# Kernel tuning notes

Hardware: AMD Instinct MI355X
Metric: run time of the kernel (lower is better)

Reference implementation:

```python
import jax, jax.numpy as jnp
import numpy as np

NUM_EXPERTS = 64
TOP_K = 2
B, S, EMB, MLP = 4, 2048, 1024, 2048


def setup_inputs() -> dict:
    key = jax.random.key(0)
    k1, k2, k3, k4, k5 = jax.random.split(key, 5)
    inputs = jax.random.normal(k1, (B, S, EMB), dtype=jnp.float32)
    gate_kernel = jax.random.normal(k2, (EMB, NUM_EXPERTS), dtype=jnp.float32) / np.sqrt(EMB)
    w0 = jax.random.normal(k3, (NUM_EXPERTS, EMB, MLP), dtype=jnp.float32) / np.sqrt(EMB)
    w1 = jax.random.normal(k4, (NUM_EXPERTS, EMB, MLP), dtype=jnp.float32) / np.sqrt(EMB)
    wo = jax.random.normal(k5, (NUM_EXPERTS, MLP, EMB), dtype=jnp.float32) / np.sqrt(MLP)
    return {"inputs": inputs, "gate_kernel": gate_kernel, "w0": w0, "w1": w1, "wo": wo}


def reference(inputs, gate_kernel, w0, w1, wo):
    b, s, e = inputs.shape
    x = inputs.reshape(b * s, e)                                  # [T, E]
    # Router (DenseGeneral gate)
    gate_logits = jnp.einsum('te,ex->tx', x, gate_kernel)         # [T, X]
    # permute(): top-k gating + sort tokens by expert
    weights, selected = jax.lax.top_k(gate_logits, TOP_K)         # [T, K]
    weights = jax.nn.softmax(weights.astype(jnp.float32), axis=-1)
    flat_experts = selected.reshape(-1)                           # [T*K]
    sort_idx = jnp.argsort(flat_experts)                          # [T*K]
    token_idx = sort_idx // TOP_K
    sorted_x = jnp.take(x, token_idx, axis=0)                     # [T*K, E]
    group_sizes = jnp.bincount(flat_experts, length=NUM_EXPERTS).astype(jnp.int32)
    # grouped GEMMs (gated FFN: silu(x@w0) * (x@w1) @ wo)
    h0 = jax.lax.ragged_dot(sorted_x, w0, group_sizes)            # [T*K, M]
    h1 = jax.lax.ragged_dot(sorted_x, w1, group_sizes)            # [T*K, M]
    inter = jax.nn.silu(h0) * h1
    out_sorted = jax.lax.ragged_dot(inter, wo, group_sizes)       # [T*K, E]
    # unpermute(): restore token order, weighted combine over top-k
    unsorted = jnp.take(out_sorted, jnp.argsort(sort_idx), axis=0)
    per_tok = unsorted.reshape(b * s, TOP_K, e)
    out = jnp.einsum('BKE,BK->BE', per_tok.astype(jnp.float32), weights)
    return out.reshape(b, s, e)
```

## Files before the change

### kernel.cpp

```cpp
#include <hip/hip_runtime.h>
#include <hip/hip_bf16.h>
#include <math.h>

#define NTOK   8192
#define NEXP   64
#define EMBD   1024
#define MLPD   2048
#define TOPK   2
#define NFLAT  (NTOK * TOPK)
#define BKD    32
#define MAXCH  8

typedef __attribute__((ext_vector_type(4)))  float  f32x4;
typedef __attribute__((ext_vector_type(16))) float  f32x16;
typedef __attribute__((ext_vector_type(8)))  __bf16 bf16x8;

__device__ __forceinline__ void gl16(const void* g, void* lds_base) {
  __builtin_amdgcn_global_load_lds(
      (const __attribute__((address_space(1))) unsigned int*)g,
      (__attribute__((address_space(3))) unsigned int*)lds_base, 16, 0, 0);
}

#define OFF_COUNTS 0
#define OFF_BASE   256
#define OFF_RUN    512
#define OFF_EFLAT  1024
#define OFF_WFLAT  (1024 + 65536)
#define OFF_ROWTOK (1024 + 2 * 65536)
#define OFF_F2R    (1024 + 3 * 65536)
#define OFF_INTER  (1024 + 4 * 65536)
#define OFF_OS     (OFF_INTER + (size_t)NFLAT * MLPD * 2)
#define OFF_XB     OFF_OS
#define NEED_F32   (OFF_OS + (size_t)NFLAT * EMBD * 4)

__global__ __launch_bounds__(256) void cvt_x_k(const float* __restrict__ x,
                                               __bf16* __restrict__ xb) {
  size_t i = ((size_t)blockIdx.x * 256 + threadIdx.x) * 8;
  f32x4 f0 = *(const f32x4*)(x + i);
  f32x4 f1 = *(const f32x4*)(x + i + 4);
  bf16x8 v;
  #pragma unroll
  for (int q = 0; q < 4; ++q) { v[q] = (__bf16)f0[q]; v[4 + q] = (__bf16)f1[q]; }
  *(bf16x8*)(xb + i) = v;
}

__global__ __launch_bounds__(256) void router_topk(
    const float* __restrict__ x, const float* __restrict__ gk,
    int* __restrict__ e_flat, float* __restrict__ w_flat) {
  int t = blockIdx.x * 4 + (threadIdx.x >> 6);
  int l = threadIdx.x & 63;
  const float* xr = x + (size_t)t * EMBD;
  float acc = 0.f;
  #pragma unroll 8
  for (int i = 0; i < EMBD; ++i)
    acc = fmaf(xr[i], gk[i * NEXP + l], acc);
  float m = acc;
  for (int o = 32; o; o >>= 1) m = fmaxf(m, __shfl_xor(m, o));
  unsigned long long b1 = __ballot(acc == m);
  int i1 = __ffsll(b1) - 1;
  float v2 = (l == i1) ? -INFINITY : acc;
  float m2 = v2;
  for (int o = 32; o; o >>= 1) m2 = fmaxf(m2, __shfl_xor(m2, o));
  unsigned long long b2 = __ballot(v2 == m2);
  int i2 = __ffsll(b2) - 1;
  if (l == 0) {
    float e2 = expf(m2 - m);
    float inv = 1.f / (1.f + e2);
    e_flat[2 * t] = i1;  e_flat[2 * t + 1] = i2;
    w_flat[2 * t] = inv; w_flat[2 * t + 1] = e2 * inv;
  }
}

__global__ void hist_k(const int* __restrict__ ef, int* __restrict__ counts) {
  int j = blockIdx.x * 256 + threadIdx.x;
  if (j < NFLAT) atomicAdd(&counts[ef[j]], 1);
}

__global__ void scan_k(const int* __restrict__ counts, int* __restrict__ base) {
  if (threadIdx.x == 0) {
    int s = 0;
    for (int e = 0; e < NEXP; ++e) { base[e] = s; s += counts[e]; }
  }
}

__global__ void scatter_k(const int* __restrict__ ef, const int* __restrict__ base,
                          int* __restrict__ run, int* __restrict__ rowtok,
                          int* __restrict__ f2r) {
  int j = blockIdx.x * 256 + threadIdx.x;
  if (j < NFLAT) {
    int e = ef[j];
    int r = base[e] + atomicAdd(&run[e], 1);
    f2r[j] = r;
    rowtok[r] = j >> 1;
  }
}

__global__ __launch_bounds__(256, 2) void gemm1_k(
    const __bf16* __restrict__ xb, const float* __restrict__ w0,
    const float* __restrict__ w1, const int* __restrict__ counts,
    const int* __restrict__ base, const int* __restrict__ rowtok,
    __hip_bfloat16* __restrict__ inter) {
  int e = blockIdx.z;
  int Me = counts[e];
  int mc = blockIdx.y;
  if (mc * 128 >= Me) return;
  int rs = base[e];
  int nb = blockIdx.x * 64;
  int t = threadIdx.x;
  int wv = t >> 6, l = t & 63;
  int wr = wv >> 1, wc = wv & 1;
  int lo = l & 31, hi = l >> 5;

  __shared__ __bf16 A1[3][4096];
  __shared__ float  B1[3][4096];

  int rga = mc * 128 + wv * 32 + lo; rga = rga < Me ? rga : Me - 1;
  const __bf16* abase = xb + (size_t)rowtok[rs + rga] * EMBD + hi * 8;
  int bm = wv >> 1, bk0 = (wv & 1) * 16;
  const float* wsel = bm ? w1 : w0;
  const float* wbase = wsel + (size_t)e * EMBD * MLPD + nb + (l & 15) * 4 +
                       (size_t)(l >> 4) * MLPD;

  auto STAGE = [&](int ks, int buf) {
    int kk = ks * BKD;
    #pragma unroll
    for (int kh = 0; kh < 2; ++kh)
      gl16(abase + kk + kh * 16, &A1[buf][(wv * 2 + kh) * 512]);
    #pragma unroll
    for (int j = 0; j < 4; ++j)
      gl16(wbase + (size_t)(kk + bk0 + j * 4) * MLPD,
           &B1[buf][bm * 2048 + (bk0 + j * 4) * 64]);
  };

  f32x16 acc0[2], acc1[2];
  #pragma unroll
  for (int g = 0; g < 2; ++g)
    #pragma unroll
    for (int r = 0; r < 16; ++r) { acc0[g][r] = 0.f; acc1[g][r] = 0.f; }

  const int NT = EMBD / BKD;
  STAGE(0, 0);
  STAGE(1, 1);
  int bufR = 0, bufW = 2;
  for (int ks = 0; ks < NT; ++ks) {
    if (ks + 1 < NT) asm volatile("s_waitcnt vmcnt(6)" ::: "memory");
    else             asm volatile("s_waitcnt vmcnt(0)" ::: "memory");
    __builtin_amdgcn_sched_barrier(0);
    __builtin_amdgcn_s_barrier();
    if (ks + 2 < NT) STAGE(ks + 2, bufW);

    bf16x8 av[2][2];
    #pragma unroll
    for (int g = 0; g < 2; ++g)
      #pragma unroll
      for (int kh = 0; kh < 2; ++kh)
        av[g][kh] = *(const bf16x8*)&A1[bufR][((wr * 2 + g) * 2 + kh) * 512 + l * 8];
    float b[2][2][8];
    #pragma unroll
    for (int m = 0; m < 2; ++m)
      #pragma unroll
      for (int kh = 0; kh < 2; ++kh) {
        int bi = m * 2048 + (kh * 16 + hi * 8) * 64 + wc * 32 + lo;
        #pragma unroll
        for (int q = 0; q < 8; ++q) b[m][kh][q] = B1[bufR][bi + q * 64];
      }
    bf16x8 bv0[2], bv1[2];
    #pragma unroll
    for (int kh = 0; kh < 2; ++kh)
      #pragma unroll
      for (int q = 0; q < 8; ++q) {
        bv0[kh][q] = (__bf16)b[0][kh][q];
        bv1[kh][q] = (__bf16)b[1][kh][q];
      }
    #pragma unroll
    for (int kh = 0; kh < 2; ++kh)
      #pragma unroll
      for (int g = 0; g < 2; ++g) {
        acc0[g] = __builtin_amdgcn_mfma_f32_32x32x16_bf16(av[g][kh], bv0[kh], acc0[g], 0, 0, 0);
        acc1[g] = __builtin_amdgcn_mfma_f32_32x32x16_bf16(av[g][kh], bv1[kh], acc1[g], 0, 0, 0);
      }
    bufR = bufR == 2 ? 0 : bufR + 1;
    bufW = bufW == 2 ? 0 : bufW + 1;
  }

  #pragma unroll
  for (int g = 0; g < 2; ++g)
    #pragma unroll
    for (int r = 0; r < 16; ++r) {
      int rl = mc * 128 + wr * 64 + g * 32 + (r & 3) + 8 * (r >> 2) + 4 * hi;
      if (rl < Me) {
        float h0 = acc0[g][r], h1 = acc1[g][r];
        float s = h0 / (1.f + expf(-h0)) * h1;
        inter[(size_t)(rs + rl) * MLPD + nb + wc * 32 + lo] = (__hip_bfloat16)s;
      }
    }
}

template <typename OS_T>
__global__ __launch_bounds__(256, 3) void gemm2_k(
    const __hip_bfloat16* __restrict__ inter, const float* __restrict__ wo,
    const int* __restrict__ counts, const int* __restrict__ base,
    OS_T* __restrict__ os) {
  int e = blockIdx.z;
  int Me = counts[e];
  int mc = blockIdx.y;
  if (mc * 128 >= Me) return;
  int rs = base[e];
  int nb = blockIdx.x * 64;
  int t = threadIdx.x;
  int wv = t >> 6, l = t & 63;
  int wr = wv >> 1, wc = wv & 1;
  int lo = l & 31, hi = l >> 5;

  __shared__ __bf16 A2[3][4096];
  __shared__ float  B2[3][2048];

  int rga = mc * 128 + wv * 32 + lo; rga = rga < Me ? rga : Me - 1;
  const __bf16* abase = (const __bf16*)inter + (size_t)(rs + rga) * MLPD + hi * 8;
  const float* wbase = wo + (size_t)e * MLPD * EMBD + nb + (l & 15) * 4 +
                       (size_t)(l >> 4) * EMBD;

  auto STAGE = [&](int ks, int buf) {
    int kk = ks * BKD;
    #pragma unroll
    for (int kh = 0; kh < 2; ++kh)
      gl16(abase + kk + kh * 16, &A2[buf][(wv * 2 + kh) * 512]);
    #pragma unroll
    for (int j = 0; j < 2; ++j)
      gl16(wbase + (size_t)(kk + wv * 8 + j * 4) * EMBD,
           &B2[buf][(wv * 8 + j * 4) * 64]);
  };

  f32x16 acc[2];
  #pragma unroll
  for (int g = 0; g < 2; ++g)
    #pragma unroll
    for (int r = 0; r < 16; ++r) acc[g][r] = 0.f;

  const int NT = MLPD / BKD;
  STAGE(0, 0);
  STAGE(1, 1);
  int bufR = 0, bufW = 2;
  for (int ks = 0; ks < NT; ++ks) {
    if (ks + 1 < NT) asm volatile("s_waitcnt vmcnt(4)" ::: "memory");
    else             asm volatile("s_waitcnt vmcnt(0)" ::: "memory");
    __builtin_amdgcn_sched_barrier(0);
    __builtin_amdgcn_s_barrier();
    if (ks + 2 < NT) STAGE(ks + 2, bufW);

    bf16x8 av[2][2];
    #pragma unroll
    for (int g = 0; g < 2; ++g)
      #pragma unroll
      for (int kh = 0; kh < 2; ++kh)
        av[g][kh] = *(const bf16x8*)&A2[bufR][((wr * 2 + g) * 2 + kh) * 512 + l * 8];
    float b[2][8];
    #pragma unroll
    for (int kh = 0; kh < 2; ++kh) {
      int bi = (kh * 16 + hi * 8) * 64 + wc * 32 + lo;
      #pragma unroll
      for (int q = 0; q < 8; ++q) b[kh][q] = B2[bufR][bi + q * 64];
    }
    bf16x8 bv[2];
    #pragma unroll
    for (int kh = 0; kh < 2; ++kh)
      #pragma unroll
      for (int q = 0; q < 8; ++q) bv[kh][q] = (__bf16)b[kh][q];
    #pragma unroll
    for (int kh = 0; kh < 2; ++kh)
      #pragma unroll
      for (int g = 0; g < 2; ++g)
        acc[g] = __builtin_amdgcn_mfma_f32_32x32x16_bf16(av[g][kh], bv[kh], acc[g], 0, 0, 0);
    bufR = bufR == 2 ? 0 : bufR + 1;
    bufW = bufW == 2 ? 0 : bufW + 1;
  }

  #pragma unroll
  for (int g = 0; g < 2; ++g)
    #pragma unroll
    for (int r = 0; r < 16; ++r) {
      int rl = mc * 128 + wr * 64 + g * 32 + (r & 3) + 8 * (r >> 2) + 4 * hi;
      if (rl < Me)
        os[(size_t)(rs + rl) * EMBD + nb + wc * 32 + lo] = (OS_T)acc[g][r];
    }
}

template <typename OS_T>
__global__ __launch_bounds__(256) void combine_k(
    const OS_T* __restrict__ os, const int* __restrict__ f2r,
    const float* __restrict__ wf, float* __restrict__ out) {
  int t = blockIdx.x;
  int c = threadIdx.x * 4;
  int r0 = f2r[2 * t], r1 = f2r[2 * t + 1];
  float wa = wf[2 * t], wb = wf[2 * t + 1];
  const OS_T* pa = os + (size_t)r0 * EMBD + c;
  const OS_T* pb = os + (size_t)r1 * EMBD + c;
  float4 o;
  o.x = wa * (float)pa[0] + wb * (float)pb[0];
  o.y = wa * (float)pa[1] + wb * (float)pb[1];
  o.z = wa * (float)pa[2] + wb * (float)pb[2];
  o.w = wa * (float)pa[3] + wb * (float)pb[3];
  *(float4*)(out + (size_t)t * EMBD + c) = o;
}

extern "C" void kernel_launch(void* const* d_in, const int* in_sizes, int n_in,
                              void* d_out, int out_size, void* d_ws, size_t ws_size,
                              hipStream_t stream) {
  const float* x  = (const float*)d_in[0];
  const float* gk = (const float*)d_in[1];
  const float* w0 = (const float*)d_in[2];
  const float* w1 = (const float*)d_in[3];
  const float* wo = (const float*)d_in[4];
  float* out = (float*)d_out;
  char* ws = (char*)d_ws;

  int*   counts = (int*)(ws + OFF_COUNTS);
  int*   basep  = (int*)(ws + OFF_BASE);
  int*   run    = (int*)(ws + OFF_RUN);
  int*   ef     = (int*)(ws + OFF_EFLAT);
  float* wfl    = (float*)(ws + OFF_WFLAT);
  int*   rowtok = (int*)(ws + OFF_ROWTOK);
  int*   f2r    = (int*)(ws + OFF_F2R);
  __hip_bfloat16* inter = (__hip_bfloat16*)(ws + OFF_INTER);
  __bf16* xb = (__bf16*)(ws + OFF_XB);

  hipMemsetAsync(ws, 0, 1024, stream);
  cvt_x_k<<<NTOK * EMBD / (256 * 8), 256, 0, stream>>>(x, xb);
  router_topk<<<NTOK / 4, 256, 0, stream>>>(x, gk, ef, wfl);
  hist_k<<<NFLAT / 256, 256, 0, stream>>>(ef, counts);
  scan_k<<<1, 64, 0, stream>>>(counts, basep);
  scatter_k<<<NFLAT / 256, 256, 0, stream>>>(ef, basep, run, rowtok, f2r);
  gemm1_k<<<dim3(MLPD / 64, MAXCH, NEXP), 256, 0, stream>>>(xb, w0, w1, counts, basep, rowtok, inter);

  if (ws_size >= NEED_F32) {
    float* os = (float*)(ws + OFF_OS);
    gemm2_k<float><<<dim3(EMBD / 64, MAXCH, NEXP), 256, 0, stream>>>(inter, wo, counts, basep, os);
    combine_k<float><<<NTOK, 256, 0, stream>>>(os, f2r, wfl, out);
  } else {
    __hip_bfloat16* os = (__hip_bfloat16*)(ws + OFF_OS);
    gemm2_k<__hip_bfloat16><<<dim3(EMBD / 64, MAXCH, NEXP), 256, 0, stream>>>(inter, wo, counts, basep, os);
    combine_k<__hip_bfloat16><<<NTOK, 256, 0, stream>>>(os, f2r, wfl, out);
  }
}
```

Measured before the change: 938.0 us.

## Convert fp32 expert weights to bf16 in registers before LDS store in GEMMs

Both grouped GEMM kernels stop copying fp32 weight tiles straight into LDS and converting them on every read. They now load the weights into registers, convert them to bf16 and write them to LDS in an MFMA-ready packed layout. Fragments are then read with single 16-byte LDS loads instead of eight scalar strided reads plus conversions. This halves the LDS footprint for B, which allows higher occupancy targets (launch bounds raised to 3 and 4), at the cost of extra register staging and an lgkmcnt wait in the pipeline.

```diff
diff --git a/kernel.cpp b/kernel.cpp
--- a/kernel.cpp
+++ b/kernel.cpp
@@ -12,8 +12,10 @@
 #define MAXCH  8
 
 typedef __attribute__((ext_vector_type(4)))  float  f32x4;
+typedef __attribute__((ext_vector_type(2)))  float  f32x2;
 typedef __attribute__((ext_vector_type(16))) float  f32x16;
 typedef __attribute__((ext_vector_type(8)))  __bf16 bf16x8;
+typedef __attribute__((ext_vector_type(4)))  __bf16 bf16x4;
 
 __device__ __forceinline__ void gl16(const void* g, void* lds_base) {
   __builtin_amdgcn_global_load_lds(
@@ -95,7 +97,7 @@
   }
 }
 
-__global__ __launch_bounds__(256, 2) void gemm1_k(
+__global__ __launch_bounds__(256, 3) void gemm1_k(
     const __bf16* __restrict__ xb, const float* __restrict__ w0,
     const float* __restrict__ w1, const int* __restrict__ counts,
     const int* __restrict__ base, const int* __restrict__ rowtok,
@@ -111,25 +113,36 @@
   int wr = wv >> 1, wc = wv & 1;
   int lo = l & 31, hi = l >> 5;
 
-  __shared__ __bf16 A1[3][4096];
-  __shared__ float  B1[3][4096];
+  __shared__ __bf16 Ax[3][4096];
+  __shared__ __bf16 Bx[3][4096];
 
   int rga = mc * 128 + wv * 32 + lo; rga = rga < Me ? rga : Me - 1;
   const __bf16* abase = xb + (size_t)rowtok[rs + rga] * EMBD + hi * 8;
-  int bm = wv >> 1, bk0 = (wv & 1) * 16;
-  const float* wsel = bm ? w1 : w0;
-  const float* wbase = wsel + (size_t)e * EMBD * MLPD + nb + (l & 15) * 4 +
-                       (size_t)(l >> 4) * MLPD;
-
-  auto STAGE = [&](int ks, int buf) {
+  int bm = t >> 7, ko = (t >> 5) & 3, np = t & 31;
+  const float* bgb = (bm ? w1 : w0) + (size_t)e * EMBD * MLPD + nb + np * 2;
+  int n0 = np * 2;
+  int bslot = ((bm * 2 + (ko >> 1)) * 2 + (n0 >> 5)) * 64 + (ko & 1) * 32 + (n0 & 31);
+
+  f32x2 vb[8];
+
+  auto LOADB = [&](int ks) {
     int kk = ks * BKD;
     #pragma unroll
-    for (int kh = 0; kh < 2; ++kh)
-      gl16(abase + kk + kh * 16, &A1[buf][(wv * 2 + kh) * 512]);
-    #pragma unroll
-    for (int j = 0; j < 4; ++j)
-      gl16(wbase + (size_t)(kk + bk0 + j * 4) * MLPD,
-           &B1[buf][bm * 2048 + (bk0 + j * 4) * 64]);
+    for (int j = 0; j < 8; ++j)
+      vb[j] = *(const f32x2*)(bgb + (size_t)(kk + ko * 8 + j) * MLPD);
+  };
+  auto WRITEB = [&](int buf) {
+    bf16x8 c0, c1;
+    #pragma unroll
+    for (int j = 0; j < 8; ++j) { c0[j] = (__bf16)vb[j][0]; c1[j] = (__bf16)vb[j][1]; }
+    *(bf16x8*)&Bx[buf][bslot * 8]     = c0;
+    *(bf16x8*)&Bx[buf][bslot * 8 + 8] = c1;
+  };
+  auto STAGEA = [&](int ks, int buf) {
+    int kk = ks * BKD;
+    #pragma unroll
+    for (int kh = 0; kh < 2; ++kh)
+      gl16(abase + kk + kh * 16, &Ax[buf][(wv * 2 + kh) * 512]);
   };
 
   f32x16 acc0[2], acc1[2];
@@ -139,39 +152,40 @@
     for (int r = 0; r < 16; ++r) { acc0[g][r] = 0.f; acc1[g][r] = 0.f; }
 
   const int NT = EMBD / BKD;
-  STAGE(0, 0);
-  STAGE(1, 1);
-  int bufR = 0, bufW = 2;
+  LOADB(0);
+  asm volatile("s_waitcnt vmcnt(0)" ::: "memory");
+  WRITEB(0);
+  LOADB(1);
+  __builtin_amdgcn_sched_barrier(0);
+  STAGEA(0, 0);
+  STAGEA(1, 1);
+
   for (int ks = 0; ks < NT; ++ks) {
-    if (ks + 1 < NT) asm volatile("s_waitcnt vmcnt(6)" ::: "memory");
+    int cur = ks % 3;
+    if (ks + 1 < NT) asm volatile("s_waitcnt vmcnt(2)" ::: "memory");
     else             asm volatile("s_waitcnt vmcnt(0)" ::: "memory");
     __builtin_amdgcn_sched_barrier(0);
+    asm volatile("s_waitcnt lgkmcnt(0)" ::: "memory");
+    __builtin_amdgcn_sched_barrier(0);
     __builtin_amdgcn_s_barrier();
-    if (ks + 2 < NT) STAGE(ks + 2, bufW);
-
-    bf16x8 av[2][2];
+    if (ks + 1 < NT) WRITEB((ks + 1) % 3);
+    __builtin_amdgcn_sched_barrier(0);
+    if (ks + 2 < NT) LOADB(ks + 2);
+    __builtin_amdgcn_sched_barrier(0);
+    if (ks + 2 < NT) STAGEA(ks + 2, (ks + 2) % 3);
+    __builtin_amdgcn_sched_barrier(0);
+
+    bf16x8 av[2][2], bv0[2], bv1[2];
     #pragma unroll
     for (int g = 0; g < 2; ++g)
       #pragma unroll
       for (int kh = 0; kh < 2; ++kh)
-        av[g][kh] = *(const bf16x8*)&A1[bufR][((wr * 2 + g) * 2 + kh) * 512 + l * 8];
-    float b[2][2][8];
-    #pragma unroll
-    for (int m = 0; m < 2; ++m)
-      #pragma unroll
-      for (int kh = 0; kh < 2; ++kh) {
-        int bi = m * 2048 + (kh * 16 + hi * 8) * 64 + wc * 32 + lo;
-        #pragma unroll
-        for (int q = 0; q < 8; ++q) b[m][kh][q] = B1[bufR][bi + q * 64];
-      }
-    bf16x8 bv0[2], bv1[2];
-    #pragma unroll
-    for (int kh = 0; kh < 2; ++kh)
-      #pragma unroll
-      for (int q = 0; q < 8; ++q) {
-        bv0[kh][q] = (__bf16)b[0][kh][q];
-        bv1[kh][q] = (__bf16)b[1][kh][q];
-      }
+        av[g][kh] = *(const bf16x8*)&Ax[cur][((wr * 2 + g) * 2 + kh) * 512 + l * 8];
+    #pragma unroll
+    for (int kh = 0; kh < 2; ++kh) {
+      bv0[kh] = *(const bf16x8*)&Bx[cur][((0 + kh) * 2 + wc) * 512 + l * 8];
+      bv1[kh] = *(const bf16x8*)&Bx[cur][((2 + kh) * 2 + wc) * 512 + l * 8];
+    }
     #pragma unroll
     for (int kh = 0; kh < 2; ++kh)
       #pragma unroll
@@ -179,8 +193,6 @@
         acc0[g] = __builtin_amdgcn_mfma_f32_32x32x16_bf16(av[g][kh], bv0[kh], acc0[g], 0, 0, 0);
         acc1[g] = __builtin_amdgcn_mfma_f32_32x32x16_bf16(av[g][kh], bv1[kh], acc1[g], 0, 0, 0);
       }
-    bufR = bufR == 2 ? 0 : bufR + 1;
-    bufW = bufW == 2 ? 0 : bufW + 1;
   }
 
   #pragma unroll
@@ -197,7 +209,7 @@
 }
 
 template <typename OS_T>
-__global__ __launch_bounds__(256, 3) void gemm2_k(
+__global__ __launch_bounds__(256, 4) void gemm2_k(
     const __hip_bfloat16* __restrict__ inter, const float* __restrict__ wo,
     const int* __restrict__ counts, const int* __restrict__ base,
     OS_T* __restrict__ os) {
@@ -212,23 +224,37 @@
   int wr = wv >> 1, wc = wv & 1;
   int lo = l & 31, hi = l >> 5;
 
-  __shared__ __bf16 A2[3][4096];
-  __shared__ float  B2[3][2048];
+  __shared__ __bf16 Ax[3][4096];
+  __shared__ __bf16 Bx[3][2048];
 
   int rga = mc * 128 + wv * 32 + lo; rga = rga < Me ? rga : Me - 1;
   const __bf16* abase = (const __bf16*)inter + (size_t)(rs + rga) * MLPD + hi * 8;
-  const float* wbase = wo + (size_t)e * MLPD * EMBD + nb + (l & 15) * 4 +
-                       (size_t)(l >> 4) * EMBD;
-
-  auto STAGE = [&](int ks, int buf) {
+  int kq = t >> 5, np = t & 31;
+  const float* bgb = wo + (size_t)e * MLPD * EMBD + nb + np * 2;
+  int n0 = np * 2;
+  int bslot = ((kq >> 2) * 2 + (n0 >> 5)) * 64 + ((kq >> 1) & 1) * 32 + (n0 & 31);
+  int qo = (kq & 1) * 4;
+
+  f32x2 vb[4];
+
+  auto LOADB = [&](int ks) {
     int kk = ks * BKD;
     #pragma unroll
-    for (int kh = 0; kh < 2; ++kh)
-      gl16(abase + kk + kh * 16, &A2[buf][(wv * 2 + kh) * 512]);
-    #pragma unroll
-    for (int j = 0; j < 2; ++j)
-      gl16(wbase + (size_t)(kk + wv * 8 + j * 4) * EMBD,
-           &B2[buf][(wv * 8 + j * 4) * 64]);
+    for (int j = 0; j < 4; ++j)
+      vb[j] = *(const f32x2*)(bgb + (size_t)(kk + kq * 4 + j) * EMBD);
+  };
+  auto WRITEB = [&](int buf) {
+    bf16x4 c0, c1;
+    #pragma unroll
+    for (int j = 0; j < 4; ++j) { c0[j] = (__bf16)vb[j][0]; c1[j] = (__bf16)vb[j][1]; }
+    *(bf16x4*)&Bx[buf][bslot * 8 + qo]     = c0;
+    *(bf16x4*)&Bx[buf][bslot * 8 + 8 + qo] = c1;
+  };
+  auto STAGEA = [&](int ks, int buf) {
+    int kk = ks * BKD;
+    #pragma unroll
+    for (int kh = 0; kh < 2; ++kh)
+      gl16(abase + kk + kh * 16, &Ax[buf][(wv * 2 + kh) * 512]);
   };
 
   f32x16 acc[2];
@@ -238,41 +264,43 @@
     for (int r = 0; r < 16; ++r) acc[g][r] = 0.f;
 
   const int NT = MLPD / BKD;
-  STAGE(0, 0);
-  STAGE(1, 1);
-  int bufR = 0, bufW = 2;
+  LOADB(0);
+  asm volatile("s_waitcnt vmcnt(0)" ::: "memory");
+  WRITEB(0);
+  LOADB(1);
+  __builtin_amdgcn_sched_barrier(0);
+  STAGEA(0, 0);
+  STAGEA(1, 1);
+
   for (int ks = 0; ks < NT; ++ks) {
-    if (ks + 1 < NT) asm volatile("s_waitcnt vmcnt(4)" ::: "memory");
+    int cur = ks % 3;
+    if (ks + 1 < NT) asm volatile("s_waitcnt vmcnt(2)" ::: "memory");
     else             asm volatile("s_waitcnt vmcnt(0)" ::: "memory");
     __builtin_amdgcn_sched_barrier(0);
+    asm volatile("s_waitcnt lgkmcnt(0)" ::: "memory");
+    __builtin_amdgcn_sched_barrier(0);
     __builtin_amdgcn_s_barrier();
-    if (ks + 2 < NT) STAGE(ks + 2, bufW);
-
-    bf16x8 av[2][2];
+    if (ks + 1 < NT) WRITEB((ks + 1) % 3);
+    __builtin_amdgcn_sched_barrier(0);
+    if (ks + 2 < NT) LOADB(ks + 2);
+    __builtin_amdgcn_sched_barrier(0);
+    if (ks + 2 < NT) STAGEA(ks + 2, (ks + 2) % 3);
+    __builtin_amdgcn_sched_barrier(0);
+
+    bf16x8 av[2][2], bv[2];
     #pragma unroll
     for (int g = 0; g < 2; ++g)
       #pragma unroll
       for (int kh = 0; kh < 2; ++kh)
-        av[g][kh] = *(const bf16x8*)&A2[bufR][((wr * 2 + g) * 2 + kh) * 512 + l * 8];
-    float b[2][8];
-    #pragma unroll
-    for (int kh = 0; kh < 2; ++kh) {
-      int bi = (kh * 16 + hi * 8) * 64 + wc * 32 + lo;
-      #pragma unroll
-      for (int q = 0; q < 8; ++q) b[kh][q] = B2[bufR][bi + q * 64];
-    }
-    bf16x8 bv[2];
-    #pragma unroll
-    for (int kh = 0; kh < 2; ++kh)
-      #pragma unroll
-      for (int q = 0; q < 8; ++q) bv[kh][q] = (__bf16)b[kh][q];
+        av[g][kh] = *(const bf16x8*)&Ax[cur][((wr * 2 + g) * 2 + kh) * 512 + l * 8];
+    #pragma unroll
+    for (int kh = 0; kh < 2; ++kh)
+      bv[kh] = *(const bf16x8*)&Bx[cur][(kh * 2 + wc) * 512 + l * 8];
     #pragma unroll
     for (int kh = 0; kh < 2; ++kh)
       #pragma unroll
       for (int g = 0; g < 2; ++g)
         acc[g] = __builtin_amdgcn_mfma_f32_32x32x16_bf16(av[g][kh], bv[kh], acc[g], 0, 0, 0);
-    bufR = bufR == 2 ? 0 : bufR + 1;
-    bufW = bufW == 2 ? 0 : bufW + 1;
   }
 
   #pragma unroll
```

After: 944.9 us. Within noise of the previous version (+0.7%).

## Give each wave private LDS tiles and stage weights through registers as bf16

Applied to the files above, without the earlier changes.

Both grouped GEMM kernels now give every wave its own double-buffered LDS region. The fp32 weight tiles are loaded into registers, converted to bf16 and written to LDS already in MFMA operand layout. This removes the block-wide s_barrier per k-step and the per-element fp32 LDS reads and conversions in the inner loop, and it halves LDS footprint for B. The cost is redundant A and B loads across waves that used to share a tile, a register-prefetch pipeline with hand-tuned vmcnt counts, and the risk that the waitcnt accounting or cross-lane LDS visibility without a barrier is wrong.

```diff
diff --git a/kernel.cpp b/kernel.cpp
--- a/kernel.cpp
+++ b/kernel.cpp
@@ -12,6 +12,7 @@
 #define MAXCH  8
 
 typedef __attribute__((ext_vector_type(4)))  float  f32x4;
+typedef __attribute__((ext_vector_type(2)))  float  f32x2;
 typedef __attribute__((ext_vector_type(16))) float  f32x16;
 typedef __attribute__((ext_vector_type(8)))  __bf16 bf16x8;
 
@@ -111,27 +112,23 @@
   int wr = wv >> 1, wc = wv & 1;
   int lo = l & 31, hi = l >> 5;
 
-  __shared__ __bf16 A1[3][4096];
-  __shared__ float  B1[3][4096];
-
-  int rga = mc * 128 + wv * 32 + lo; rga = rga < Me ? rga : Me - 1;
-  const __bf16* abase = xb + (size_t)rowtok[rs + rga] * EMBD + hi * 8;
-  int bm = wv >> 1, bk0 = (wv & 1) * 16;
-  const float* wsel = bm ? w1 : w0;
-  const float* wbase = wsel + (size_t)e * EMBD * MLPD + nb + (l & 15) * 4 +
-                       (size_t)(l >> 4) * MLPD;
-
-  auto STAGE = [&](int ks, int buf) {
-    int kk = ks * BKD;
-    #pragma unroll
-    for (int kh = 0; kh < 2; ++kh)
-      gl16(abase + kk + kh * 16, &A1[buf][(wv * 2 + kh) * 512]);
-    #pragma unroll
-    for (int j = 0; j < 4; ++j)
-      gl16(wbase + (size_t)(kk + bk0 + j * 4) * MLPD,
-           &B1[buf][bm * 2048 + (bk0 + j * 4) * 64]);
-  };
-
+  __shared__ __bf16 sh[4][2][4096];
+  __bf16* Aw[2] = { &sh[wv][0][0],    &sh[wv][1][0] };
+  __bf16* Bw[2] = { &sh[wv][0][2048], &sh[wv][1][2048] };
+
+  const __bf16* abase[2];
+  #pragma unroll
+  for (int g = 0; g < 2; ++g) {
+    int rga = mc * 128 + wr * 64 + g * 32 + lo;
+    rga = rga < Me ? rga : Me - 1;
+    abase[g] = xb + (size_t)rowtok[rs + rga] * EMBD + hi * 8;
+  }
+  int r4 = l >> 4, c0 = 2 * (l & 15);
+  int bmat = r4 >> 1, bkh = (r4 & 1) * 16;
+  const float* bgb = (bmat ? w1 : w0) + (size_t)e * EMBD * MLPD + nb + wc * 32 + c0;
+  int bslot = r4 * 512;
+
+  f32x2 vbA[16], vbB[16];
   f32x16 acc0[2], acc1[2];
   #pragma unroll
   for (int g = 0; g < 2; ++g)
@@ -139,49 +136,73 @@
     for (int r = 0; r < 16; ++r) { acc0[g][r] = 0.f; acc1[g][r] = 0.f; }
 
   const int NT = EMBD / BKD;
-  STAGE(0, 0);
-  STAGE(1, 1);
-  int bufR = 0, bufW = 2;
-  for (int ks = 0; ks < NT; ++ks) {
-    if (ks + 1 < NT) asm volatile("s_waitcnt vmcnt(6)" ::: "memory");
-    else             asm volatile("s_waitcnt vmcnt(0)" ::: "memory");
-    __builtin_amdgcn_sched_barrier(0);
-    __builtin_amdgcn_s_barrier();
-    if (ks + 2 < NT) STAGE(ks + 2, bufW);
-
-    bf16x8 av[2][2];
-    #pragma unroll
-    for (int g = 0; g < 2; ++g)
-      #pragma unroll
-      for (int kh = 0; kh < 2; ++kh)
-        av[g][kh] = *(const bf16x8*)&A1[bufR][((wr * 2 + g) * 2 + kh) * 512 + l * 8];
-    float b[2][2][8];
-    #pragma unroll
-    for (int m = 0; m < 2; ++m)
-      #pragma unroll
-      for (int kh = 0; kh < 2; ++kh) {
-        int bi = m * 2048 + (kh * 16 + hi * 8) * 64 + wc * 32 + lo;
-        #pragma unroll
-        for (int q = 0; q < 8; ++q) b[m][kh][q] = B1[bufR][bi + q * 64];
-      }
-    bf16x8 bv0[2], bv1[2];
-    #pragma unroll
-    for (int kh = 0; kh < 2; ++kh)
-      #pragma unroll
-      for (int q = 0; q < 8; ++q) {
-        bv0[kh][q] = (__bf16)b[0][kh][q];
-        bv1[kh][q] = (__bf16)b[1][kh][q];
-      }
-    #pragma unroll
-    for (int kh = 0; kh < 2; ++kh)
-      #pragma unroll
-      for (int g = 0; g < 2; ++g) {
-        acc0[g] = __builtin_amdgcn_mfma_f32_32x32x16_bf16(av[g][kh], bv0[kh], acc0[g], 0, 0, 0);
-        acc1[g] = __builtin_amdgcn_mfma_f32_32x32x16_bf16(av[g][kh], bv1[kh], acc1[g], 0, 0, 0);
-      }
-    bufR = bufR == 2 ? 0 : bufR + 1;
-    bufW = bufW == 2 ? 0 : bufW + 1;
-  }
+
+#define LOADB1(VB, KS)                                                  \
+  { int kkc = (KS) * BKD; kkc = kkc < EMBD ? kkc : EMBD - BKD;          \
+    _Pragma("unroll")                                                   \
+    for (int q = 0; q < 16; ++q)                                        \
+      VB[q] = *(const f32x2*)(bgb + (size_t)(kkc + bkh + q) * MLPD); }
+#define WRITEB1(VB, BUF)                                                \
+  { bf16x8 p0, p1, p2, p3;                                              \
+    _Pragma("unroll")                                                   \
+    for (int q = 0; q < 8; ++q) {                                       \
+      p0[q] = (__bf16)VB[q][0];     p1[q] = (__bf16)VB[8 + q][0];       \
+      p2[q] = (__bf16)VB[q][1];     p3[q] = (__bf16)VB[8 + q][1];       \
+    }                                                                   \
+    *(bf16x8*)&Bw[BUF][bslot + (c0) * 8]          = p0;                 \
+    *(bf16x8*)&Bw[BUF][bslot + (32 + c0) * 8]     = p1;                 \
+    *(bf16x8*)&Bw[BUF][bslot + (c0 + 1) * 8]      = p2;                 \
+    *(bf16x8*)&Bw[BUF][bslot + (32 + c0 + 1) * 8] = p3; }
+#define STAGEA1(KS, BUF)                                                \
+  { int kkc = (KS) * BKD; kkc = kkc < EMBD ? kkc : EMBD - BKD;          \
+    _Pragma("unroll")                                                   \
+    for (int g = 0; g < 2; ++g)                                         \
+      _Pragma("unroll")                                                 \
+      for (int kh = 0; kh < 2; ++kh)                                    \
+        gl16(abase[g] + kkc + kh * 16, Aw[BUF] + (g * 2 + kh) * 512); }
+#define COMPUTE1(BUF)                                                   \
+  { bf16x8 av[2][2], bv0[2], bv1[2];                                    \
+    _Pragma("unroll")                                                   \
+    for (int g = 0; g < 2; ++g)                                         \
+      _Pragma("unroll")                                                 \
+      for (int kh = 0; kh < 2; ++kh)                                    \
+        av[g][kh] = *(const bf16x8*)&Aw[BUF][(g * 2 + kh) * 512 + l * 8]; \
+    _Pragma("unroll")                                                   \
+    for (int kh = 0; kh < 2; ++kh) {                                    \
+      bv0[kh] = *(const bf16x8*)&Bw[BUF][(0 + kh) * 512 + l * 8];       \
+      bv1[kh] = *(const bf16x8*)&Bw[BUF][(2 + kh) * 512 + l * 8];       \
+    }                                                                   \
+    _Pragma("unroll")                                                   \
+    for (int kh = 0; kh < 2; ++kh)                                      \
+      _Pragma("unroll")                                                 \
+      for (int g = 0; g < 2; ++g) {                                     \
+        acc0[g] = __builtin_amdgcn_mfma_f32_32x32x16_bf16(av[g][kh], bv0[kh], acc0[g], 0, 0, 0); \
+        acc1[g] = __builtin_amdgcn_mfma_f32_32x32x16_bf16(av[g][kh], bv1[kh], acc1[g], 0, 0, 0); \
+      } }
+#define G1_ITER(J, SETC, SETO)                                          \
+  { LOADB1(SETC, (J) + 2);                                              \
+    STAGEA1((J) + 1, ((J) + 1) & 1);                                    \
+    asm volatile("s_waitcnt vmcnt(20)" ::: "memory");                   \
+    __builtin_amdgcn_sched_barrier(0);                                  \
+    WRITEB1(SETO, ((J) + 1) & 1);                                       \
+    COMPUTE1((J) & 1); }
+
+  LOADB1(vbA, 0);
+  asm volatile("s_waitcnt vmcnt(0)" ::: "memory");
+  WRITEB1(vbA, 0);
+  LOADB1(vbB, 1);
+  STAGEA1(0, 0);
+
+  for (int j = 0; j < NT; j += 2) {
+    G1_ITER(j, vbA, vbB);
+    G1_ITER(j + 1, vbB, vbA);
+  }
+  asm volatile("s_waitcnt vmcnt(0)" ::: "memory");
+#undef G1_ITER
+#undef COMPUTE1
+#undef STAGEA1
+#undef WRITEB1
+#undef LOADB1
 
   #pragma unroll
   for (int g = 0; g < 2; ++g)
@@ -212,25 +233,23 @@
   int wr = wv >> 1, wc = wv & 1;
   int lo = l & 31, hi = l >> 5;
 
-  __shared__ __bf16 A2[3][4096];
-  __shared__ float  B2[3][2048];
-
-  int rga = mc * 128 + wv * 32 + lo; rga = rga < Me ? rga : Me - 1;
-  const __bf16* abase = (const __bf16*)inter + (size_t)(rs + rga) * MLPD + hi * 8;
-  const float* wbase = wo + (size_t)e * MLPD * EMBD + nb + (l & 15) * 4 +
-                       (size_t)(l >> 4) * EMBD;
-
-  auto STAGE = [&](int ks, int buf) {
-    int kk = ks * BKD;
-    #pragma unroll
-    for (int kh = 0; kh < 2; ++kh)
-      gl16(abase + kk + kh * 16, &A2[buf][(wv * 2 + kh) * 512]);
-    #pragma unroll
-    for (int j = 0; j < 2; ++j)
-      gl16(wbase + (size_t)(kk + wv * 8 + j * 4) * EMBD,
-           &B2[buf][(wv * 8 + j * 4) * 64]);
-  };
-
+  __shared__ __bf16 sh[4][2][3072];
+  __bf16* Aw[2] = { &sh[wv][0][0],    &sh[wv][1][0] };
+  __bf16* Bw[2] = { &sh[wv][0][2048], &sh[wv][1][2048] };
+
+  const __bf16* abase[2];
+  #pragma unroll
+  for (int g = 0; g < 2; ++g) {
+    int rga = mc * 128 + wr * 64 + g * 32 + lo;
+    rga = rga < Me ? rga : Me - 1;
+    abase[g] = (const __bf16*)inter + (size_t)(rs + rga) * MLPD + hi * 8;
+  }
+  int r4 = l >> 4, c0 = 2 * (l & 15);
+  int bko = (r4 >> 1) * 16 + (r4 & 1) * 8;
+  const float* bgb = wo + (size_t)e * MLPD * EMBD + nb + wc * 32 + c0;
+  int bkh_slot = (r4 >> 1) * 512, boct = (r4 & 1) * 32;
+
+  f32x2 vbA[8], vbB[8];
   f32x16 acc[2];
   #pragma unroll
   for (int g = 0; g < 2; ++g)
@@ -238,42 +257,64 @@
     for (int r = 0; r < 16; ++r) acc[g][r] = 0.f;
 
   const int NT = MLPD / BKD;
-  STAGE(0, 0);
-  STAGE(1, 1);
-  int bufR = 0, bufW = 2;
-  for (int ks = 0; ks < NT; ++ks) {
-    if (ks + 1 < NT) asm volatile("s_waitcnt vmcnt(4)" ::: "memory");
-    else             asm volatile("s_waitcnt vmcnt(0)" ::: "memory");
-    __builtin_amdgcn_sched_barrier(0);
-    __builtin_amdgcn_s_barrier();
-    if (ks + 2 < NT) STAGE(ks + 2, bufW);
-
-    bf16x8 av[2][2];
-    #pragma unroll
-    for (int g = 0; g < 2; ++g)
-      #pragma unroll
-      for (int kh = 0; kh < 2; ++kh)
-        av[g][kh] = *(const bf16x8*)&A2[bufR][((wr * 2 + g) * 2 + kh) * 512 + l * 8];
-    float b[2][8];
-    #pragma unroll
-    for (int kh = 0; kh < 2; ++kh) {
-      int bi = (kh * 16 + hi * 8) * 64 + wc * 32 + lo;
-      #pragma unroll
-      for (int q = 0; q < 8; ++q) b[kh][q] = B2[bufR][bi + q * 64];
-    }
-    bf16x8 bv[2];
-    #pragma unroll
-    for (int kh = 0; kh < 2; ++kh)
-      #pragma unroll
-      for (int q = 0; q < 8; ++q) bv[kh][q] = (__bf16)b[kh][q];
-    #pragma unroll
-    for (int kh = 0; kh < 2; ++kh)
-      #pragma unroll
-      for (int g = 0; g < 2; ++g)
-        acc[g] = __builtin_amdgcn_mfma_f32_32x32x16_bf16(av[g][kh], bv[kh], acc[g], 0, 0, 0);
-    bufR = bufR == 2 ? 0 : bufR + 1;
-    bufW = bufW == 2 ? 0 : bufW + 1;
-  }
+
+#define LOADB2(VB, KS)                                                  \
+  { int kkc = (KS) * BKD; kkc = kkc < MLPD ? kkc : MLPD - BKD;          \
+    _Pragma("unroll")                                                   \
+    for (int q = 0; q < 8; ++q)                                         \
+      VB[q] = *(const f32x2*)(bgb + (size_t)(kkc + bko + q) * EMBD); }
+#define WRITEB2(VB, BUF)                                                \
+  { bf16x8 p0, p1;                                                      \
+    _Pragma("unroll")                                                   \
+    for (int q = 0; q < 8; ++q) { p0[q] = (__bf16)VB[q][0]; p1[q] = (__bf16)VB[q][1]; } \
+    *(bf16x8*)&Bw[BUF][bkh_slot + (boct + c0) * 8]     = p0;            \
+    *(bf16x8*)&Bw[BUF][bkh_slot + (boct + c0 + 1) * 8] = p1; }
+#define STAGEA2(KS, BUF)                                                \
+  { int kkc = (KS) * BKD; kkc = kkc < MLPD ? kkc : MLPD - BKD;          \
+    _Pragma("unroll")                                                   \
+    for (int g = 0; g < 2; ++g)                                         \
+      _Pragma("unroll")                                                 \
+      for (int kh = 0; kh < 2; ++kh)                                    \
+        gl16(abase[g] + kkc + kh * 16, Aw[BUF] + (g * 2 + kh) * 512); }
+#define COMPUTE2(BUF)                                                   \
+  { bf16x8 av[2][2], bv[2];                                             \
+    _Pragma("unroll")                                                   \
+    for (int g = 0; g < 2; ++g)                                         \
+      _Pragma("unroll")                                                 \
+      for (int kh = 0; kh < 2; ++kh)                                    \
+        av[g][kh] = *(const bf16x8*)&Aw[BUF][(g * 2 + kh) * 512 + l * 8]; \
+    _Pragma("unroll")                                                   \
+    for (int kh = 0; kh < 2; ++kh)                                      \
+      bv[kh] = *(const bf16x8*)&Bw[BUF][kh * 512 + l * 8];              \
+    _Pragma("unroll")                                                   \
+    for (int kh = 0; kh < 2; ++kh)                                      \
+      _Pragma("unroll")                                                 \
+      for (int g = 0; g < 2; ++g)                                       \
+        acc[g] = __builtin_amdgcn_mfma_f32_32x32x16_bf16(av[g][kh], bv[kh], acc[g], 0, 0, 0); }
+#define G2_ITER(J, SETC, SETO)                                          \
+  { LOADB2(SETC, (J) + 2);                                              \
+    STAGEA2((J) + 1, ((J) + 1) & 1);                                    \
+    asm volatile("s_waitcnt vmcnt(12)" ::: "memory");                   \
+    __builtin_amdgcn_sched_barrier(0);                                  \
+    WRITEB2(SETO, ((J) + 1) & 1);                                       \
+    COMPUTE2((J) & 1); }
+
+  LOADB2(vbA, 0);
+  asm volatile("s_waitcnt vmcnt(0)" ::: "memory");
+  WRITEB2(vbA, 0);
+  LOADB2(vbB, 1);
+  STAGEA2(0, 0);
+
+  for (int j = 0; j < NT; j += 2) {
+    G2_ITER(j, vbA, vbB);
+    G2_ITER(j + 1, vbB, vbA);
+  }
+  asm volatile("s_waitcnt vmcnt(0)" ::: "memory");
+#undef G2_ITER
+#undef COMPUTE2
+#undef STAGEA2
+#undef WRITEB2
+#undef LOADB2
 
   #pragma unroll
   for (int g = 0; g < 2; ++g)
```

New measurement: 1.461 ms. +55.8%, slower.
